# Kernel tuning notes

Hardware: AMD Instinct MI355X
Metric: run time of the kernel (lower is better)

Reference implementation:

```python
import jax, jax.numpy as jnp
import numpy as np

TEMP = 0.07
EPS = 1e-12  # matches torch F.normalize default eps


def _l2norm(x):
    n = jnp.sqrt(jnp.sum(x * x, axis=-1, keepdims=True))
    return x / jnp.maximum(n, EPS)


def setup_inputs() -> dict:
    key = jax.random.key(0)
    kq, kk = jax.random.split(key)
    N, D = 16384, 256
    q = jax.random.normal(kq, (N, D), dtype=jnp.float32)
    k = jax.random.normal(kk, (N, D), dtype=jnp.float32)
    return {"q": q, "k": k}


def reference(q, k):
    qn = _l2norm(q)
    kn = _l2norm(k)
    logits = (qn @ kn.T) / TEMP            # [N, N]
    # cross-entropy with labels = arange(N): mean over rows of (logsumexp - diag)
    lse = jax.nn.logsumexp(logits, axis=-1)  # [N]
    diag = jnp.diagonal(logits)              # [N]
    return jnp.mean(lse - diag)
```

## Files before the change

kernel.cpp:

```cpp
#include <hip/hip_runtime.h>
#include <hip/hip_bf16.h>
#include <cstdint>
#include <cstddef>

#define NROWS 16384
#define DDIM  256
#define SPLITS 16
#define NTILES 256

typedef __attribute__((ext_vector_type(4))) float f32x4;
typedef __attribute__((ext_vector_type(4))) float fl4;
typedef __attribute__((ext_vector_type(4))) int   i32x4;
typedef __attribute__((ext_vector_type(8))) int   i32x8;

constexpr float SCALE_EXP2 = 20.609929155556627f;
constexpr float LN2F       = 0.69314718055994531f;
constexpr float INV_T      = 14.285714285714286f;

__device__ inline void gload_lds16(const void* g, void* l) {
  __builtin_amdgcn_global_load_lds(
      (const __attribute__((address_space(1))) void*)g,
      (__attribute__((address_space(3))) void*)l, 16, 0, 0);
}

__global__ __launch_bounds__(256) void norm_kernel(
    const float* __restrict__ q, const float* __restrict__ k,
    unsigned char* __restrict__ qn, unsigned char* __restrict__ kn,
    float* __restrict__ diag, float* __restrict__ rowsum,
    float* __restrict__ out)
{
  const int wave = threadIdx.x >> 6, lane = threadIdx.x & 63;
  const int row = blockIdx.x * 4 + wave;
  const size_t off = (size_t)row * DDIM + lane * 4;

  fl4 vq = *(const fl4*)(q + off);
  fl4 vk = *(const fl4*)(k + off);
  float ssq = vq.x * vq.x + vq.y * vq.y + vq.z * vq.z + vq.w * vq.w;
  float ssk = vk.x * vk.x + vk.y * vk.y + vk.z * vk.z + vk.w * vk.w;
  float dot = vq.x * vk.x + vq.y * vk.y + vq.z * vk.z + vq.w * vk.w;
#pragma unroll
  for (int m = 1; m < 64; m <<= 1) {
    ssq += __shfl_xor(ssq, m, 64);
    ssk += __shfl_xor(ssk, m, 64);
    dot += __shfl_xor(dot, m, 64);
  }
  float rq = 1.0f / fmaxf(sqrtf(ssq), 1e-12f);
  float rk = 1.0f / fmaxf(sqrtf(ssk), 1e-12f);

  float sq = rq * SCALE_EXP2;
  int pq = __builtin_amdgcn_cvt_pk_fp8_f32(vq.x * sq, vq.y * sq, 0, false);
  pq     = __builtin_amdgcn_cvt_pk_fp8_f32(vq.z * sq, vq.w * sq, pq, true);
  *(int*)(qn + off) = pq;
  int pk = __builtin_amdgcn_cvt_pk_fp8_f32(vk.x * rk, vk.y * rk, 0, false);
  pk     = __builtin_amdgcn_cvt_pk_fp8_f32(vk.z * rk, vk.w * rk, pk, true);
  *(int*)(kn + off) = pk;

  if (lane == 0) {
    diag[row]   = dot * rq * rk * INV_T;
    rowsum[row] = 0.0f;
    if (row == 0) out[0] = 0.0f;
  }
}

__global__ __launch_bounds__(256) void lse_kernel(
    const unsigned char* __restrict__ qn, const unsigned char* __restrict__ kn,
    float* __restrict__ rowsum)
{
  __shared__ __attribute__((aligned(16))) unsigned char Bs[2][64 * DDIM];

  const int tid  = threadIdx.x;
  const int wave = tid >> 6, lane = tid & 63;
  const int l15  = lane & 15, quad = lane >> 4;
  const int split = blockIdx.x % SPLITS;
  const int rb    = blockIdx.x / SPLITS;
  const int wrow  = rb * 256 + wave * 64;
  const int t0 = (split * NTILES) / SPLITS;
  const int t1 = ((split + 1) * NTILES) / SPLITS;

  const int Ln = tid >> 4, Ljj = tid & 15;
  const int Lj = Ljj ^ Ln;
  const size_t src_off = (size_t)Ln * DDIM + (size_t)Lj * 16;

  i32x8 A[4][2];
#pragma unroll
  for (int s = 0; s < 4; ++s) {
    const unsigned char* ap = qn + (size_t)(wrow + s * 16 + l15) * DDIM + quad * 32;
#pragma unroll
    for (int ks = 0; ks < 2; ++ks)
      A[s][ks] = *(const i32x8*)(ap + ks * 128);
  }

  float sums[4][4];
#pragma unroll
  for (int s = 0; s < 4; ++s)
#pragma unroll
    for (int r = 0; r < 4; ++r) sums[s][r] = 0.0f;

  {
    const unsigned char* kbase = kn + (size_t)t0 * 64 * DDIM + src_off;
#pragma unroll
    for (int i = 0; i < 4; ++i)
      gload_lds16(kbase + i * 4096, (void*)(Bs[0] + tid * 16 + i * 4096));
  }

  for (int ct = t0; ct < t1; ++ct) {
    const int cur = (ct - t0) & 1;
    __builtin_amdgcn_s_waitcnt(0);
    __syncthreads();
    if (ct + 1 < t1) {
      const unsigned char* kbase = kn + (size_t)(ct + 1) * 64 * DDIM + src_off;
#pragma unroll
      for (int i = 0; i < 4; ++i)
        gload_lds16(kbase + i * 4096, (void*)(Bs[cur ^ 1] + tid * 16 + i * 4096));
    }

#pragma unroll
    for (int cs = 0; cs < 4; ++cs) {
      int n  = cs * 16 + l15;
      int nb = n & 15;
      const unsigned char* brow = Bs[cur] + n * DDIM;
      f32x4 acc0 = {0.f, 0.f, 0.f, 0.f};
      f32x4 acc1 = {0.f, 0.f, 0.f, 0.f};
      f32x4 acc2 = {0.f, 0.f, 0.f, 0.f};
      f32x4 acc3 = {0.f, 0.f, 0.f, 0.f};
#pragma unroll
      for (int ks = 0; ks < 2; ++ks) {
        int c0 = ks * 8 + quad * 2;
        i32x4 lo = *(const i32x4*)(brow + ((c0 ^ nb) * 16));
        i32x4 hi = *(const i32x4*)(brow + (((c0 + 1) ^ nb) * 16));
        i32x8 b = {lo.x, lo.y, lo.z, lo.w, hi.x, hi.y, hi.z, hi.w};
        acc0 = __builtin_amdgcn_mfma_scale_f32_16x16x128_f8f6f4(A[0][ks], b, acc0, 0, 0, 0, 127, 0, 127);
        acc1 = __builtin_amdgcn_mfma_scale_f32_16x16x128_f8f6f4(A[1][ks], b, acc1, 0, 0, 0, 127, 0, 127);
        acc2 = __builtin_amdgcn_mfma_scale_f32_16x16x128_f8f6f4(A[2][ks], b, acc2, 0, 0, 0, 127, 0, 127);
        acc3 = __builtin_amdgcn_mfma_scale_f32_16x16x128_f8f6f4(A[3][ks], b, acc3, 0, 0, 0, 127, 0, 127);
      }
#pragma unroll
      for (int r = 0; r < 4; ++r) {
        sums[0][r] += __builtin_amdgcn_exp2f(acc0[r]);
        sums[1][r] += __builtin_amdgcn_exp2f(acc1[r]);
        sums[2][r] += __builtin_amdgcn_exp2f(acc2[r]);
        sums[3][r] += __builtin_amdgcn_exp2f(acc3[r]);
      }
    }
  }

#pragma unroll
  for (int s = 0; s < 4; ++s)
#pragma unroll
    for (int r = 0; r < 4; ++r) {
      float v = sums[s][r];
      v += __shfl_xor(v, 1, 64);
      v += __shfl_xor(v, 2, 64);
      v += __shfl_xor(v, 4, 64);
      v += __shfl_xor(v, 8, 64);
      if (l15 == 0) atomicAdd(&rowsum[wrow + s * 16 + quad * 4 + r], v);
    }
}

__global__ void final_kernel(const float* __restrict__ rowsum,
                             const float* __restrict__ diag,
                             float* __restrict__ out)
{
  int row = blockIdx.x * 256 + threadIdx.x;
  float c = __builtin_amdgcn_logf(rowsum[row]) * LN2F - diag[row];
#pragma unroll
  for (int m = 1; m < 64; m <<= 1) c += __shfl_xor(c, m, 64);
  __shared__ float red[4];
  int wave = threadIdx.x >> 6, lane = threadIdx.x & 63;
  if (lane == 0) red[wave] = c;
  __syncthreads();
  if (threadIdx.x == 0) {
    float s = red[0] + red[1] + red[2] + red[3];
    atomicAdd(out, s * (1.0f / NROWS));
  }
}

extern "C" void kernel_launch(void* const* d_in, const int* in_sizes, int n_in,
                              void* d_out, int out_size, void* d_ws, size_t ws_size,
                              hipStream_t stream)
{
  const float* q = (const float*)d_in[0];
  const float* k = (const float*)d_in[1];
  float* out = (float*)d_out;

  char* ws = (char*)d_ws;
  unsigned char* qn = (unsigned char*)ws;
  unsigned char* kn = (unsigned char*)(ws + (4u << 20));
  float* diag   = (float*)(ws + (8u << 20));
  float* rowsum = (float*)(ws + (8u << 20) + (64u << 10));

  norm_kernel <<<NROWS / 4, 256, 0, stream>>>(q, k, qn, kn, diag, rowsum, out);
  lse_kernel  <<<(NROWS / 256) * SPLITS, 256, 0, stream>>>(qn, kn, rowsum);
  final_kernel<<<NROWS / 256, 256, 0, stream>>>(rowsum, diag, out);
}
```

Baseline: 140.9 us.

## Fuse final reduction into LSE kernel via per-row completion counters

Removes the separate final kernel launch. Each row now carries an atomic counter, and the last split to finish a row computes log(rowsum) minus diag and atomically adds it to the output. It also precomputes the swizzled LDS offsets once instead of recomputing XORs inside the loop. The trade is one kernel launch removed against many extra atomics: 16 per row, plus one output atomic per row, all contending on a single address.

```diff
diff --git a/kernel.cpp b/kernel.cpp
--- a/kernel.cpp
+++ b/kernel.cpp
@@ -27,7 +27,7 @@
     const float* __restrict__ q, const float* __restrict__ k,
     unsigned char* __restrict__ qn, unsigned char* __restrict__ kn,
     float* __restrict__ diag, float* __restrict__ rowsum,
-    float* __restrict__ out)
+    int* __restrict__ cnt, float* __restrict__ out)
 {
   const int wave = threadIdx.x >> 6, lane = threadIdx.x & 63;
   const int row = blockIdx.x * 4 + wave;
@@ -58,13 +58,15 @@
   if (lane == 0) {
     diag[row]   = dot * rq * rk * INV_T;
     rowsum[row] = 0.0f;
+    cnt[row]    = 0;
     if (row == 0) out[0] = 0.0f;
   }
 }
 
 __global__ __launch_bounds__(256) void lse_kernel(
     const unsigned char* __restrict__ qn, const unsigned char* __restrict__ kn,
-    float* __restrict__ rowsum)
+    float* __restrict__ rowsum, const float* __restrict__ diag,
+    int* __restrict__ cnt, float* __restrict__ out)
 {
   __shared__ __attribute__((aligned(16))) unsigned char Bs[2][64 * DDIM];
 
@@ -80,6 +82,11 @@
   const int Ln = tid >> 4, Ljj = tid & 15;
   const int Lj = Ljj ^ Ln;
   const size_t src_off = (size_t)Ln * DDIM + (size_t)Lj * 16;
+
+  const int o00 = ((quad * 2    ) ^ l15) * 16;
+  const int o01 = ((quad * 2 + 1) ^ l15) * 16;
+  const int o10 = ((quad * 2 + 8) ^ l15) * 16;
+  const int o11 = ((quad * 2 + 9) ^ l15) * 16;
 
   i32x8 A[4][2];
 #pragma unroll
@@ -114,20 +121,17 @@
         gload_lds16(kbase + i * 4096, (void*)(Bs[cur ^ 1] + tid * 16 + i * 4096));
     }
 
+    const unsigned char* brow = Bs[cur] + l15 * DDIM;
 #pragma unroll
-    for (int cs = 0; cs < 4; ++cs) {
-      int n  = cs * 16 + l15;
-      int nb = n & 15;
-      const unsigned char* brow = Bs[cur] + n * DDIM;
+    for (int cs = 0; cs < 4; ++cs, brow += 16 * DDIM) {
       f32x4 acc0 = {0.f, 0.f, 0.f, 0.f};
       f32x4 acc1 = {0.f, 0.f, 0.f, 0.f};
       f32x4 acc2 = {0.f, 0.f, 0.f, 0.f};
       f32x4 acc3 = {0.f, 0.f, 0.f, 0.f};
 #pragma unroll
       for (int ks = 0; ks < 2; ++ks) {
-        int c0 = ks * 8 + quad * 2;
-        i32x4 lo = *(const i32x4*)(brow + ((c0 ^ nb) * 16));
-        i32x4 hi = *(const i32x4*)(brow + (((c0 + 1) ^ nb) * 16));
+        i32x4 lo = *(const i32x4*)(brow + (ks ? o10 : o00));
+        i32x4 hi = *(const i32x4*)(brow + (ks ? o11 : o01));
         i32x8 b = {lo.x, lo.y, lo.z, lo.w, hi.x, hi.y, hi.z, hi.w};
         acc0 = __builtin_amdgcn_mfma_scale_f32_16x16x128_f8f6f4(A[0][ks], b, acc0, 0, 0, 0, 127, 0, 127);
         acc1 = __builtin_amdgcn_mfma_scale_f32_16x16x128_f8f6f4(A[1][ks], b, acc1, 0, 0, 0, 127, 0, 127);
@@ -155,23 +159,21 @@
       v += __shfl_xor(v, 8, 64);
       if (l15 == 0) atomicAdd(&rowsum[wrow + s * 16 + quad * 4 + r], v);
     }
-}
-
-__global__ void final_kernel(const float* __restrict__ rowsum,
-                             const float* __restrict__ diag,
-                             float* __restrict__ out)
-{
-  int row = blockIdx.x * 256 + threadIdx.x;
-  float c = __builtin_amdgcn_logf(rowsum[row]) * LN2F - diag[row];
+  __threadfence();
+  if (l15 == 0) {
 #pragma unroll
-  for (int m = 1; m < 64; m <<= 1) c += __shfl_xor(c, m, 64);
-  __shared__ float red[4];
-  int wave = threadIdx.x >> 6, lane = threadIdx.x & 63;
-  if (lane == 0) red[wave] = c;
-  __syncthreads();
-  if (threadIdx.x == 0) {
-    float s = red[0] + red[1] + red[2] + red[3];
-    atomicAdd(out, s * (1.0f / NROWS));
+    for (int s = 0; s < 4; ++s)
+#pragma unroll
+      for (int r = 0; r < 4; ++r) {
+        int row = wrow + s * 16 + quad * 4 + r;
+        int o = atomicAdd(&cnt[row], 1);
+        if (o == SPLITS - 1) {
+          __threadfence();
+          float tot = atomicAdd(&rowsum[row], 0.0f);
+          float c = __builtin_amdgcn_logf(tot) * LN2F - diag[row];
+          atomicAdd(out, c * (1.0f / NROWS));
+        }
+      }
   }
 }
 
@@ -188,8 +190,8 @@
   unsigned char* kn = (unsigned char*)(ws + (4u << 20));
   float* diag   = (float*)(ws + (8u << 20));
   float* rowsum = (float*)(ws + (8u << 20) + (64u << 10));
+  int*   cnt    = (int*)  (ws + (8u << 20) + (128u << 10));
 
-  norm_kernel <<<NROWS / 4, 256, 0, stream>>>(q, k, qn, kn, diag, rowsum, out);
-  lse_kernel  <<<(NROWS / 256) * SPLITS, 256, 0, stream>>>(qn, kn, rowsum);
-  final_kernel<<<NROWS / 256, 256, 0, stream>>>(rowsum, diag, out);
+  norm_kernel <<<NROWS / 4, 256, 0, stream>>>(q, k, qn, kn, diag, rowsum, cnt, out);
+  lse_kernel  <<<(NROWS / 256) * SPLITS, 256, 0, stream>>>(qn, kn, rowsum, diag, cnt, out);
 }
```

Result: slower. 562.7 us (+299.3%).
